# Kernel tuning notes

Measured on AMD Instinct MI355X. Metric: run time of the kernel, lower is better.

The kernel has to match this reference:

```python
import jax, jax.numpy as jnp
import numpy as np

B, L_IN, D = 8, 4096, 256
MAX_T = 2048
NOISE_SCALE = 0.1
EPS = 1e-12


def setup_inputs() -> dict:
    key = jax.random.key(0)
    kx, kl, kf = jax.random.split(key, 3)
    x = jax.random.normal(kx, (B, L_IN, D), dtype=jnp.float32)
    # variable valid input lengths -> padding_mask (True = pad)
    in_len = jax.random.randint(kl, (B,), L_IN // 2, L_IN + 1)
    padding_mask = jnp.arange(L_IN)[None, :] >= in_len[:, None]
    # variable target lengths, ensure max equals MAX_T (static output shape)
    finallength = jax.random.randint(kf, (B,), MAX_T // 2, MAX_T + 1)
    finallength = finallength.at[0].set(MAX_T)
    return {"x": x, "finallength": finallength, "padding_mask": padding_mask, "max_T": MAX_T}


def _resample(x, finallength, padding_mask, max_T):
    Bb, L_in, Dd = x.shape
    dt = x.dtype
    # compact valid tokens to the front (stable sort: False=valid sorts first,
    # preserving order) == seq = x[b, ~padding_mask[b]] padded at the back
    order = jnp.argsort(padding_mask.astype(jnp.int32), axis=1, stable=True)  # [B,L_in]
    seq = jnp.take_along_axis(x, order[:, :, None], axis=1)                    # [B,L_in,D]
    L = (~padding_mask).sum(axis=1)   # [B] valid input lengths (int)
    T = finallength                    # [B] target lengths (int)
    j = jnp.arange(max_T)              # output bins
    i = jnp.arange(L_in)               # input cells

    # --- F.interpolate(mode='area') == adaptive avg pool: integer bin boundaries
    # i0 = floor(j*L/T), i1 = ceil((j+1)*L/T) computed in exact integer arithmetic
    Tc = jnp.maximum(T, 1)[:, None]                      # [B,1]
    jL = j[None, :] * L[:, None]                          # [B,maxT]
    i0 = jL // Tc                                         # [B,maxT]
    i1 = (jL + L[:, None] + Tc - 1) // Tc                 # [B,maxT]
    Wint = ((i[None, None, :] >= i0[:, :, None]) & (i[None, None, :] < i1[:, :, None])).astype(dt)  # [B,maxT,L_in]
    valid_j = (j[None, :] < T[:, None]) & (L[:, None] > 0)  # [B,maxT] valid output bins
    Wint = Wint * valid_j[:, :, None].astype(dt)
    cnt = jnp.maximum(Wint.sum(-1, keepdims=True), 1.0)
    out = jnp.einsum('btl,bld->btd', Wint / cnt, seq)      # [B,maxT,D]

    # --- local noise: exact weighted per-bin std via fractional overlaps
    Lf = L.astype(dt)
    Tf = jnp.maximum(T, 1).astype(dt)
    step = Lf / Tf                                         # [B]
    start = j[None, :].astype(dt) * step[:, None]          # [B,maxT]
    end = start + step[:, None]
    ifl = i.astype(dt)
    Wfrac = jnp.clip(jnp.minimum(ifl[None, None, :] + 1.0, end[:, :, None])
                     - jnp.maximum(ifl[None, None, :], start[:, :, None]), 0.0)  # [B,maxT,L_in]
    Wfrac = Wfrac * (ifl[None, :] < Lf[:, None]).astype(dt)[:, None, :]
    Wfrac = Wfrac * valid_j[:, :, None].astype(dt)
    Wsum = jnp.maximum(Wfrac.sum(-1, keepdims=True), EPS)
    mean = jnp.einsum('btl,bld->btd', Wfrac, seq) / Wsum
    mean_sq = jnp.einsum('btl,bld->btd', Wfrac, seq * seq) / Wsum
    std = jnp.sqrt(jnp.maximum(mean_sq - mean * mean, EPS))
    eps_noise = jax.lax.stop_gradient(
        jax.random.normal(jax.random.key(42), out.shape, dtype=dt))
    out = out + eps_noise * std * NOISE_SCALE

    out = out * valid_j[:, :, None].astype(dt)             # zero padded rows
    out_mask = ~valid_j                                     # True = pad
    return out, out_mask


def reference(x, finallength, padding_mask, max_T):
    return _resample(x, finallength, padding_mask, max_T)
```

## Files before the change

### kernel.cpp

```cpp
#include <hip/hip_runtime.h>
#include <math.h>


__device__ __forceinline__ unsigned rotl32(unsigned x, unsigned r) {
  return (x << r) | (x >> (32u - r));
}

__device__ __forceinline__ void threefry2x32(unsigned ks0, unsigned ks1,
                                             unsigned& x0, unsigned& x1) {
  const unsigned ks2 = ks0 ^ ks1 ^ 0x1BD11BDAu;
  x0 += ks0; x1 += ks1;
#define TFR(r) { x0 += x1; x1 = rotl32(x1, (r)); x1 ^= x0; }
  TFR(13u) TFR(15u) TFR(26u) TFR(6u)   x0 += ks1; x1 += ks2 + 1u;
  TFR(17u) TFR(29u) TFR(16u) TFR(24u)  x0 += ks2; x1 += ks0 + 2u;
  TFR(13u) TFR(15u) TFR(26u) TFR(6u)   x0 += ks0; x1 += ks1 + 3u;
  TFR(17u) TFR(29u) TFR(16u) TFR(24u)  x0 += ks1; x1 += ks2 + 4u;
  TFR(13u) TFR(15u) TFR(26u) TFR(6u)   x0 += ks2; x1 += ks0 + 5u;
#undef TFR
}

__global__ __launch_bounds__(256) void resample_kernel(
    const float* __restrict__ x, const int* __restrict__ finallength,
    const int* __restrict__ padding_mask, float* __restrict__ out,
    float* __restrict__ out_mask, int L_in) {
  const int D = 256;
  const int wave = threadIdx.x >> 6;
  const int lane = threadIdx.x & 63;
  const int t = blockIdx.x * 4 + wave;
  const int b = blockIdx.y;
  const int maxT = gridDim.x * 4;
  const int bt = b * maxT + t;
  const size_t obase = (size_t)bt * D + lane * 4;

  const int* __restrict__ m = padding_mask + (size_t)b * L_in;
  int blo = 0, bhi = L_in;
  while (blo < bhi) {
    const int mid = (blo + bhi) >> 1;
    if (m[mid] != 0) bhi = mid; else blo = mid + 1;
  }
  const int L = blo;
  const int T = finallength[b];

  if (t >= T || L <= 0) {
    *(float4*)(out + obase) = make_float4(0.f, 0.f, 0.f, 0.f);
    if (lane == 0) out_mask[bt] = 1.0f;
    return;
  }

  const unsigned Tc = (unsigned)T;
  const unsigned jL = (unsigned)t * (unsigned)L;
  const int i0 = (int)(jL / Tc);
  const int i1 = (int)((jL + (unsigned)L + Tc - 1u) / Tc);
  const float step = (float)L / (float)Tc;
  const float start = (float)t * step;
  const float end = start + step;
  int flo = (int)floorf(start); if (flo < 0) flo = 0;
  int fhi = (int)ceilf(end);    if (fhi > L) fhi = L;
  const int lo = (i0 < flo) ? i0 : flo;
  const int hi = (i1 > fhi) ? i1 : fhi;

  float z[4];
#pragma unroll
  for (int k = 0; k < 4; ++k) {
    unsigned c0 = 0u, c1 = (unsigned)obase + (unsigned)k;
    threefry2x32(0u, 42u, c0, c1);
    const unsigned bits = c0 ^ c1;
    union { unsigned u; float f; } cvt;
    cvt.u = (bits >> 9) | 0x3F800000u;
    const float lof = -0.99999994f;
    float uu = (cvt.f - 1.0f) * 2.0f + lof;
    uu = fmaxf(lof, uu);
    z[k] = 1.41421356237309515f * erfinvf(uu);
  }

  const float4* __restrict__ xr =
      (const float4*)(x + (size_t)b * L_in * D) + lane;
  float4 sI = make_float4(0.f, 0.f, 0.f, 0.f);
  float4 sX = make_float4(0.f, 0.f, 0.f, 0.f);
  float4 sXX = make_float4(0.f, 0.f, 0.f, 0.f);
  float sW = 0.f;
  for (int i = lo; i < hi; ++i) {
    const float4 v = xr[(size_t)i * 64];
    if (i >= i0 && i < i1) {
      sI.x += v.x; sI.y += v.y; sI.z += v.z; sI.w += v.w;
    }
    float w = fminf((float)(i + 1), end) - fmaxf((float)i, start);
    w = fmaxf(w, 0.f);
    sW += w;
    sX.x += w * v.x; sX.y += w * v.y; sX.z += w * v.z; sX.w += w * v.w;
    sXX.x += w * v.x * v.x; sXX.y += w * v.y * v.y;
    sXX.z += w * v.z * v.z; sXX.w += w * v.w * v.w;
  }
  const int cd = i1 - i0;
  const float inv_cnt = 1.f / (float)((cd > 1) ? cd : 1);
  const float inv_ws = 1.f / fmaxf(sW, 1e-12f);
  float4 o;
  {
    const float mean = sX.x * inv_ws, msq = sXX.x * inv_ws;
    o.x = sI.x * inv_cnt + (z[0] * sqrtf(fmaxf(msq - mean * mean, 1e-12f))) * 0.1f;
  }
  {
    const float mean = sX.y * inv_ws, msq = sXX.y * inv_ws;
    o.y = sI.y * inv_cnt + (z[1] * sqrtf(fmaxf(msq - mean * mean, 1e-12f))) * 0.1f;
  }
  {
    const float mean = sX.z * inv_ws, msq = sXX.z * inv_ws;
    o.z = sI.z * inv_cnt + (z[2] * sqrtf(fmaxf(msq - mean * mean, 1e-12f))) * 0.1f;
  }
  {
    const float mean = sX.w * inv_ws, msq = sXX.w * inv_ws;
    o.w = sI.w * inv_cnt + (z[3] * sqrtf(fmaxf(msq - mean * mean, 1e-12f))) * 0.1f;
  }
  *(float4*)(out + obase) = o;
  if (lane == 0) out_mask[bt] = 0.0f;
}

extern "C" void kernel_launch(void* const* d_in, const int* in_sizes, int n_in,
                              void* d_out, int out_size, void* d_ws, size_t ws_size,
                              hipStream_t stream) {
  const float* x            = (const float*)d_in[0];
  const int*   finallength  = (const int*)d_in[1];
  const int*   padding_mask = (const int*)d_in[2];

  const int B    = in_sizes[1];
  const int L_in = in_sizes[2] / B;
  const int D    = in_sizes[0] / in_sizes[2];
  const int maxT = out_size / (B * (D + 1));

  float* out      = (float*)d_out;
  float* out_mask = out + (size_t)B * maxT * D;
  (void)d_ws; (void)ws_size; (void)n_in; (void)D;

  resample_kernel<<<dim3(maxT / 4, B), 256, 0, stream>>>(
      x, finallength, padding_mask, out, out_mask, L_in);
}
```

Measured before the change: 93.50 us.

## Prefetch input rows before RNG, ballot-based length search, XCD-aware block swizzle

Issues the first six row loads before the threefry/erfinv noise computation so memory latency overlaps the RNG arithmetic. Replaces the serial binary search over the padding mask with a two-level wavefront ballot scan. Also remaps block indices so neighbouring output bins land on the same XCD for L2 reuse. The cost is more registers held live for the prefetched rows, which may lower occupancy.

```diff
diff --git a/kernel.cpp b/kernel.cpp
--- a/kernel.cpp
+++ b/kernel.cpp
@@ -26,20 +26,40 @@
   const int D = 256;
   const int wave = threadIdx.x >> 6;
   const int lane = threadIdx.x & 63;
-  const int t = blockIdx.x * 4 + wave;
+  const int maxT = gridDim.x * 4;
+
+  int bx = blockIdx.x;
+  const int nbx = gridDim.x;
+  if ((nbx & 7) == 0) {
+    const int q = nbx >> 3;
+    bx = (bx & 7) * q + (bx >> 3);
+  }
+  const int t = bx * 4 + wave;
   const int b = blockIdx.y;
-  const int maxT = gridDim.x * 4;
   const int bt = b * maxT + t;
   const size_t obase = (size_t)bt * D + lane * 4;
 
   const int* __restrict__ m = padding_mask + (size_t)b * L_in;
-  int blo = 0, bhi = L_in;
-  while (blo < bhi) {
-    const int mid = (blo + bhi) >> 1;
-    if (m[mid] != 0) bhi = mid; else blo = mid + 1;
+  const int T = finallength[b];
+
+  const int stride = (L_in + 63) >> 6;
+  int p1 = (lane + 1) * stride - 1;
+  if (p1 >= L_in) p1 = L_in - 1;
+  const unsigned long long m1 = __ballot(m[p1] != 0);
+  int L = L_in;
+  if (m1 != 0ull) {
+    const int c = (int)__ffsll(m1) - 1;
+    const int base = c * stride;
+    const int cend = (base + stride < L_in) ? base + stride : L_in;
+    for (int off = 0; ; off += 64) {
+      const int p2 = base + off + lane;
+      const bool in = p2 < cend;
+      const int pc = (p2 < L_in) ? p2 : (L_in - 1);
+      const unsigned long long m2 = __ballot(in && (m[pc] != 0));
+      if (m2 != 0ull) { L = base + off + (int)__ffsll(m2) - 1; break; }
+      if (base + off + 64 >= cend) break;
+    }
   }
-  const int L = blo;
-  const int T = finallength[b];
 
   if (t >= T || L <= 0) {
     *(float4*)(out + obase) = make_float4(0.f, 0.f, 0.f, 0.f);
@@ -58,6 +78,26 @@
   int fhi = (int)ceilf(end);    if (fhi > L) fhi = L;
   const int lo = (i0 < flo) ? i0 : flo;
   const int hi = (i1 > fhi) ? i1 : fhi;
+  const int n = hi - lo;
+
+  const float4* __restrict__ xr =
+      (const float4*)(x + (size_t)b * L_in * D) + lane;
+  constexpr int PREF = 6;
+  float4 v0, v1, v2, v3, v4, v5;
+  {
+    const int k0 = lo;
+    const int k1 = lo + ((1 < n) ? 1 : 0);
+    const int k2 = lo + ((2 < n) ? 2 : 0);
+    const int k3 = lo + ((3 < n) ? 3 : 0);
+    const int k4 = lo + ((4 < n) ? 4 : 0);
+    const int k5 = lo + ((5 < n) ? 5 : 0);
+    v0 = xr[(size_t)k0 * 64];
+    v1 = xr[(size_t)k1 * 64];
+    v2 = xr[(size_t)k2 * 64];
+    v3 = xr[(size_t)k3 * 64];
+    v4 = xr[(size_t)k4 * 64];
+    v5 = xr[(size_t)k5 * 64];
+  }
 
   float z[4];
 #pragma unroll
@@ -73,24 +113,46 @@
     z[k] = 1.41421356237309515f * erfinvf(uu);
   }
 
-  const float4* __restrict__ xr =
-      (const float4*)(x + (size_t)b * L_in * D) + lane;
   float4 sI = make_float4(0.f, 0.f, 0.f, 0.f);
   float4 sX = make_float4(0.f, 0.f, 0.f, 0.f);
   float4 sXX = make_float4(0.f, 0.f, 0.f, 0.f);
   float sW = 0.f;
-  for (int i = lo; i < hi; ++i) {
-    const float4 v = xr[(size_t)i * 64];
+
+#define ACC_ROW(K, V)                                                        \
+  if ((K) < n) {                                                             \
+    const int i = lo + (K);                                                  \
+    const float4 vv = (V);                                                   \
+    if (i >= i0 && i < i1) {                                                 \
+      sI.x += vv.x; sI.y += vv.y; sI.z += vv.z; sI.w += vv.w;                \
+    }                                                                        \
+    float w = fminf((float)(i + 1), end) - fmaxf((float)i, start);           \
+    w = fmaxf(w, 0.f);                                                       \
+    sW += w;                                                                 \
+    sX.x += w * vv.x; sX.y += w * vv.y; sX.z += w * vv.z; sX.w += w * vv.w;  \
+    sXX.x += w * vv.x * vv.x; sXX.y += w * vv.y * vv.y;                      \
+    sXX.z += w * vv.z * vv.z; sXX.w += w * vv.w * vv.w;                      \
+  }
+  ACC_ROW(0, v0)
+  ACC_ROW(1, v1)
+  ACC_ROW(2, v2)
+  ACC_ROW(3, v3)
+  ACC_ROW(4, v4)
+  ACC_ROW(5, v5)
+#undef ACC_ROW
+
+  for (int i = lo + PREF; i < hi; ++i) {
+    const float4 vv = xr[(size_t)i * 64];
     if (i >= i0 && i < i1) {
-      sI.x += v.x; sI.y += v.y; sI.z += v.z; sI.w += v.w;
+      sI.x += vv.x; sI.y += vv.y; sI.z += vv.z; sI.w += vv.w;
     }
     float w = fminf((float)(i + 1), end) - fmaxf((float)i, start);
     w = fmaxf(w, 0.f);
     sW += w;
-    sX.x += w * v.x; sX.y += w * v.y; sX.z += w * v.z; sX.w += w * v.w;
-    sXX.x += w * v.x * v.x; sXX.y += w * v.y * v.y;
-    sXX.z += w * v.z * v.z; sXX.w += w * v.w * v.w;
+    sX.x += w * vv.x; sX.y += w * vv.y; sX.z += w * vv.z; sX.w += w * vv.w;
+    sXX.x += w * vv.x * vv.x; sXX.y += w * vv.y * vv.y;
+    sXX.z += w * vv.z * vv.z; sXX.w += w * vv.w * vv.w;
   }
+
   const int cd = i1 - i0;
   const float inv_cnt = 1.f / (float)((cd > 1) ? cd : 1);
   const float inv_ws = 1.f / fmaxf(sW, 1e-12f);
```

Result: no change. 93.66 us (+0.2%).
